# Kernel optimization log

Hardware: AMD Instinct MI355X
Metric: run time of the kernel (lower is better)

The kernel has to match this reference:

```python
import jax, jax.numpy as jnp
import numpy as np

MEM = 128   # mem_dim
K = 4096    # number of object keys (each an array leaf list)
L = 128     # numbers per array
STATS_CAP = 100  # number_stats list capped at 100 entries


def setup_inputs() -> dict:
    key = jax.random.key(0)
    ks = jax.random.split(key, 13)
    s = 0.05
    return {
        "numbers": jax.random.normal(ks[0], (K, L), jnp.float32),
        "w_num": jax.random.normal(ks[1], (MEM,), jnp.float32) * s,
        "b_num": jax.random.normal(ks[2], (MEM,), jnp.float32) * s,
        "W_ih": jax.random.normal(ks[3], (4 * MEM, 2 * MEM), jnp.float32) * s,
        "W_hh": jax.random.normal(ks[4], (4 * MEM, MEM), jnp.float32) * s,
        "b_ih": jax.random.normal(ks[5], (4 * MEM,), jnp.float32) * s,
        "b_hh": jax.random.normal(ks[6], (4 * MEM,), jnp.float32) * s,
        "W_fh": jax.random.normal(ks[7], (MEM, MEM), jnp.float32) * s,
        "b_fh": jax.random.normal(ks[8], (MEM,), jnp.float32) * s,
        "W_iouh": jax.random.normal(ks[9], (3 * MEM, MEM), jnp.float32) * s,
        "b_iouh": jax.random.normal(ks[10], (3 * MEM,), jnp.float32) * s,
        "W_lout": jax.random.normal(ks[11], (MEM, MEM), jnp.float32) * s,
        "b_lout": jax.random.normal(ks[12], (MEM,), jnp.float32) * s,
    }


def _normalize_numbers(x_flat):
    # Replicates embed_number's running number_stats (tie_primitives -> one shared
    # '___default___' stats list, filled in traversal order, capped at 100 entries).
    # The k-th number is normalized by mean/std over the first min(k, 100) numbers
    # (including itself); std division only when len > 3 and std not ~0.
    n = x_flat.shape[0]
    k = jnp.arange(1, n + 1, dtype=jnp.float32)
    cs = jnp.cumsum(x_flat)
    css = jnp.cumsum(x_flat * x_flat)
    cap = jnp.minimum(k, float(STATS_CAP))
    cs_c = jnp.where(k <= STATS_CAP, cs, cs[STATS_CAP - 1])
    css_c = jnp.where(k <= STATS_CAP, css, css[STATS_CAP - 1])
    mean = cs_c / cap
    var = jnp.maximum(css_c / cap - mean * mean, 0.0)
    std = jnp.sqrt(var)
    # torch impl computes stats with numpy -> no gradient flows through them
    mean = jax.lax.stop_gradient(mean)
    std = jax.lax.stop_gradient(std)
    y = x_flat - mean
    use_std = (cap > 3.0) & (std > 1e-8)
    return jnp.where(use_std, y / jnp.where(use_std, std, 1.0), y)


def _forward(numbers, w_num, b_num, W_ih, W_hh, b_ih, b_hh,
             W_fh, b_fh, W_iouh, b_iouh, W_lout, b_lout):
    # --- embed_number: per-leaf (c=0, h = Linear(1, MEM)(norm_num)) ---
    x = _normalize_numbers(numbers.reshape(-1)).reshape(K, L)
    h_num = x[..., None] * w_num + b_num  # [K, L, MEM]

    # --- embed_array: LSTMCell over each array's children; input = cat([c_child, h_child]) ---
    # child_c is always 0 for number leaves.
    def step(carry, h_t):  # h_t: [K, MEM]
        c, h = carry
        xcat = jnp.concatenate([jnp.zeros_like(h_t), h_t], axis=-1)  # [K, 2*MEM]
        gates = xcat @ W_ih.T + b_ih + h @ W_hh.T + b_hh             # [K, 4*MEM]
        i, f, g, o = jnp.split(gates, 4, axis=-1)
        c2 = jax.nn.sigmoid(f) * c + jax.nn.sigmoid(i) * jnp.tanh(g)
        h2 = jax.nn.sigmoid(o) * jnp.tanh(c2)
        return (c2, h2), None

    z = jnp.zeros((K, MEM), numbers.dtype)
    (c_arr, h_arr), _ = jax.lax.scan(step, (z, z), jnp.swapaxes(h_num, 0, 1))
    # c_arr, h_arr: [K, MEM] final states per array child of the root object

    # --- embed_object (root): child-sum Tree-LSTM gating ---
    f_g = jax.nn.sigmoid(h_arr @ W_fh.T + b_fh)             # [K, MEM]
    fc_sum = jnp.sum(f_g * c_arr, axis=0, keepdims=True)    # [1, MEM]
    hs_bar = jnp.sum(h_arr, axis=0, keepdims=True)          # [1, MEM]
    iou = hs_bar @ W_iouh.T + b_iouh
    i, o, u = jnp.split(iou, 3, axis=-1)
    c = jax.nn.sigmoid(i) * jnp.tanh(u) + fc_sum
    h = jax.nn.sigmoid(o) * jnp.tanh(c)
    h_hat = h @ W_lout.T + b_lout
    return jnp.concatenate([c, h_hat], axis=1)  # [1, 2*MEM]


def reference(numbers, w_num, b_num, W_ih, W_hh, b_ih, b_hh,
              W_fh, b_fh, W_iouh, b_iouh, W_lout, b_lout):
    return _forward(numbers, w_num, b_num, W_ih, W_hh, b_ih, b_hh,
                    W_fh, b_fh, W_iouh, b_iouh, W_lout, b_lout)
```

## Files before the change

kernel.cpp:

```cpp
#include <hip/hip_runtime.h>
#include <math.h>

#define L2E 1.4426950408889634f
#define HSTR 136
#define PRS 16

typedef __bf16 bf16x8 __attribute__((ext_vector_type(8)));
typedef float  f32x4  __attribute__((ext_vector_type(4)));

__device__ __forceinline__ float sig2(float y) {
    return __builtin_amdgcn_rcpf(1.0f + __builtin_amdgcn_exp2f(-y));
}

__global__ void prep_kernel(const float* __restrict__ numbers,
                            const float* __restrict__ w_num,
                            const float* __restrict__ b_num,
                            const float* __restrict__ W_ih,
                            const float* __restrict__ b_ih,
                            const float* __restrict__ b_hh,
                            float* __restrict__ ws_base) {
    float* fc_hs    = ws_base;
    float* mean_lut = ws_base + 256;
    float* inv_lut  = ws_base + 356;
    float* Avec     = ws_base + 456;
    float* Bvec     = ws_base + 968;

    if (blockIdx.x == 64) {
        __shared__ float sx[100];
        int tid = threadIdx.x;
        if (tid < 256) fc_hs[tid] = 0.0f;
        if (tid < 100) sx[tid] = numbers[tid];
        __syncthreads();
        if (tid < 100) {
            float s = 0.f, ss = 0.f;
            for (int j = 0; j <= tid; ++j) { float v = sx[j]; s += v; ss += v * v; }
            float cap  = (float)(tid + 1);
            float mean = s / cap;
            float var  = ss / cap - mean * mean;
            if (var < 0.f) var = 0.f;
            float sd = sqrtf(var);
            float inv = (cap > 3.0f && sd > 1e-8f) ? (1.0f / sd) : 1.0f;
            mean_lut[tid] = mean;
            inv_lut[tid]  = inv;
        }
        return;
    }
    int j    = blockIdx.x * 8 + (threadIdx.x >> 6);
    int lane = threadIdx.x & 63;
    const float* row = W_ih + j * 256 + 128;
    float r1 = row[lane], r2 = row[lane + 64];
    float a = r1 * w_num[lane] + r2 * w_num[lane + 64];
    float b = r1 * b_num[lane] + r2 * b_num[lane + 64];
    #pragma unroll
    for (int off = 32; off >= 1; off >>= 1) {
        a += __shfl_xor(a, off);
        b += __shfl_xor(b, off);
    }
    if (lane == 0) {
        float s = (j >= 256 && j < 384) ? (2.0f * L2E) : L2E;
        Avec[j] = a * s;
        Bvec[j] = (b + b_ih[j] + b_hh[j]) * s;
    }
}

__global__ __launch_bounds__(1024, 4) void lstm_kernel(
        const float* __restrict__ numbers, const float* __restrict__ W_hh,
        const float* __restrict__ W_fh,    const float* __restrict__ b_fh,
        const float* __restrict__ mean_lut, const float* __restrict__ inv_lut,
        const float* __restrict__ Avec,     const float* __restrict__ Bvec,
        float* __restrict__ fc_sum, float* __restrict__ hs_bar) {
    __shared__ unsigned short hbuf[2][16 * HSTR];
    __shared__ float xls[128 * 16];
    __shared__ float pbuf[128 * PRS];

    const int tid  = threadIdx.x;
    const int lane = tid & 63;
    const int wave = tid >> 6;
    const bool low = wave < 8;
    const int quad = lane >> 4;
    const int lcol = lane & 15;
    const int m0   = (wave & 7) * 16;
    const int r0   = blockIdx.x * 16;

    for (int i = tid; i < 16 * 128; i += 1024) {
        int row = i >> 7;
        int t   = i & 127;
        int flat = (r0 + row) * 128 + t;
        int ii = (flat < 100) ? flat : 99;
        float v = numbers[flat];
        xls[t * 16 + row] = (v - mean_lut[ii]) * inv_lut[ii];
    }
    for (int i = tid; i < 16 * HSTR; i += 1024) hbuf[0][i] = 0;

    const int g0 = low ? 0 : 1;
    const int g1 = low ? 2 : 3;
    const float s0 = L2E;
    const float s1 = low ? (2.0f * L2E) : L2E;
    bf16x8 bf[2][4];
    #pragma unroll
    for (int gi = 0; gi < 2; ++gi) {
        int g = gi ? g1 : g0;
        float sc = gi ? s1 : s0;
        #pragma unroll
        for (int kk = 0; kk < 4; ++kk) {
            const float* p = W_hh + (g * 128 + m0 + lcol) * 128 + kk * 32 + quad * 8;
            f32x4 w0 = *(const f32x4*)p;
            f32x4 w1 = *(const f32x4*)(p + 4);
            bf16x8 bt;
            #pragma unroll
            for (int q = 0; q < 4; ++q) {
                bt[q]     = (__bf16)(w0[q] * sc);
                bt[q + 4] = (__bf16)(w1[q] * sc);
            }
            bf[gi][kk] = bt;
        }
    }
    float ag[2], bg[2];
    ag[0] = Avec[g0 * 128 + m0 + lcol];  bg[0] = Bvec[g0 * 128 + m0 + lcol];
    ag[1] = Avec[g1 * 128 + m0 + lcol];  bg[1] = Bvec[g1 * 128 + m0 + lcol];

    float c[4]  = {0.f, 0.f, 0.f, 0.f};
    float hf[4] = {0.f, 0.f, 0.f, 0.f};
    __syncthreads();

    for (int t = 0; t < 128; ++t) {
        const unsigned short* hin = hbuf[t & 1];
        unsigned short* hout = hbuf[(t + 1) & 1];
        bf16x8 af[4];
        #pragma unroll
        for (int kk = 0; kk < 4; ++kk)
            af[kk] = *(const bf16x8*)(const void*)(hin + lcol * HSTR + kk * 32 + quad * 8);
        f32x4 xq = *(const f32x4*)(const void*)(xls + t * 16 + quad * 4);
        f32x4 acc[2];
        #pragma unroll
        for (int gi = 0; gi < 2; ++gi) {
            f32x4 a0;
            #pragma unroll
            for (int r = 0; r < 4; ++r) a0[r] = xq[r] * ag[gi] + bg[gi];
            #pragma unroll
            for (int kk = 0; kk < 4; ++kk)
                a0 = __builtin_amdgcn_mfma_f32_16x16x32_bf16(af[kk], bf[gi][kk], a0, 0, 0, 0);
            acc[gi] = a0;
        }
        float sf[4], so[4];
        if (low) {
            f32x4 pv;
            #pragma unroll
            for (int r = 0; r < 4; ++r) {
                float si = sig2(acc[0][r]);
                float tg = 2.0f * sig2(acc[1][r]) - 1.0f;
                pv[r] = si * tg;
            }
            *(f32x4*)(pbuf + (m0 + lcol) * PRS + quad * 4) = pv;
        } else {
            #pragma unroll
            for (int r = 0; r < 4; ++r) {
                sf[r] = sig2(acc[0][r]);
                so[r] = sig2(acc[1][r]);
            }
        }
        __syncthreads();
        if (!low) {
            f32x4 pv = *(const f32x4*)(const void*)(pbuf + (m0 + lcol) * PRS + quad * 4);
            #pragma unroll
            for (int r = 0; r < 4; ++r) {
                float c2 = sf[r] * c[r] + pv[r];
                c[r] = c2;
                float th = 2.0f * sig2(c2 * (2.0f * L2E)) - 1.0f;
                float h = so[r] * th;
                hf[r] = h;
                hout[(quad * 4 + r) * HSTR + m0 + lcol] =
                    __builtin_bit_cast(unsigned short, (__bf16)h);
            }
        }
        __syncthreads();
    }

    if (!low) {
        float v = hf[0] + hf[1] + hf[2] + hf[3];
        v += __shfl_xor(v, 16);
        v += __shfl_xor(v, 32);
        if (lane < 16) atomicAdd(&hs_bar[m0 + lane], v);
        f32x4 facc;
        {
            float bb = b_fh[m0 + lcol] * L2E;
            #pragma unroll
            for (int r = 0; r < 4; ++r) facc[r] = bb;
        }
        #pragma unroll
        for (int kk = 0; kk < 4; ++kk) {
            bf16x8 afr = *(const bf16x8*)(const void*)(hbuf[0] + lcol * HSTR + kk * 32 + quad * 8);
            const float* p = W_fh + (m0 + lcol) * 128 + kk * 32 + quad * 8;
            f32x4 w0 = *(const f32x4*)p;
            f32x4 w1 = *(const f32x4*)(p + 4);
            bf16x8 wt;
            #pragma unroll
            for (int q = 0; q < 4; ++q) {
                wt[q]     = (__bf16)(w0[q] * L2E);
                wt[q + 4] = (__bf16)(w1[q] * L2E);
            }
            facc = __builtin_amdgcn_mfma_f32_16x16x32_bf16(afr, wt, facc, 0, 0, 0);
        }
        float fcv = 0.f;
        #pragma unroll
        for (int r = 0; r < 4; ++r) fcv += sig2(facc[r]) * c[r];
        fcv += __shfl_xor(fcv, 16);
        fcv += __shfl_xor(fcv, 32);
        if (lane < 16) atomicAdd(&fc_sum[m0 + lane], fcv);
    }
}

__global__ void finalize_kernel(const float* __restrict__ fc_sum,
                                const float* __restrict__ hs_bar,
                                const float* __restrict__ W_iouh,
                                const float* __restrict__ b_iouh,
                                const float* __restrict__ W_lout,
                                const float* __restrict__ b_lout,
                                float* __restrict__ out) {
    __shared__ float hsb[128], iou[384], hfin[128];
    int tid = threadIdx.x;
    if (tid < 128) hsb[tid] = hs_bar[tid];
    __syncthreads();
    if (tid < 384) {
        float s = b_iouh[tid];
        const f32x4* row = (const f32x4*)(W_iouh + tid * 128);
        #pragma unroll 8
        for (int m = 0; m < 32; ++m) {
            f32x4 w = row[m];
            s += w[0] * hsb[4*m] + w[1] * hsb[4*m+1] + w[2] * hsb[4*m+2] + w[3] * hsb[4*m+3];
        }
        iou[tid] = s;
    }
    __syncthreads();
    if (tid < 128) {
        float i = iou[tid], o = iou[128 + tid], u = iou[256 + tid];
        float cf = sig2(i * L2E) * (2.0f * sig2(u * 2.0f * L2E) - 1.0f) + fc_sum[tid];
        out[tid] = cf;
        hfin[tid] = sig2(o * L2E) * (2.0f * sig2(cf * 2.0f * L2E) - 1.0f);
    }
    __syncthreads();
    if (tid < 128) {
        float s = b_lout[tid];
        const f32x4* row = (const f32x4*)(W_lout + tid * 128);
        #pragma unroll 8
        for (int m = 0; m < 32; ++m) {
            f32x4 w = row[m];
            s += w[0] * hfin[4*m] + w[1] * hfin[4*m+1] + w[2] * hfin[4*m+2] + w[3] * hfin[4*m+3];
        }
        out[128 + tid] = s;
    }
}

extern "C" void kernel_launch(void* const* d_in, const int* in_sizes, int n_in,
                              void* d_out, int out_size, void* d_ws, size_t ws_size,
                              hipStream_t stream) {
    const float* numbers = (const float*)d_in[0];
    const float* w_num   = (const float*)d_in[1];
    const float* b_num   = (const float*)d_in[2];
    const float* W_ih    = (const float*)d_in[3];
    const float* W_hh    = (const float*)d_in[4];
    const float* b_ih    = (const float*)d_in[5];
    const float* b_hh    = (const float*)d_in[6];
    const float* W_fh    = (const float*)d_in[7];
    const float* b_fh    = (const float*)d_in[8];
    const float* W_iouh  = (const float*)d_in[9];
    const float* b_iouh  = (const float*)d_in[10];
    const float* W_lout  = (const float*)d_in[11];
    const float* b_lout  = (const float*)d_in[12];
    float* out = (float*)d_out;

    float* ws       = (float*)d_ws;
    float* fc_sum   = ws;
    float* hs_bar   = ws + 128;
    float* mean_lut = ws + 256;
    float* inv_lut  = ws + 356;
    float* Avec     = ws + 456;
    float* Bvec     = ws + 968;

    prep_kernel<<<65, 512, 0, stream>>>(numbers, w_num, b_num, W_ih, b_ih, b_hh, ws);
    lstm_kernel<<<256, 1024, 0, stream>>>(numbers, W_hh, W_fh, b_fh,
                                          mean_lut, inv_lut, Avec, Bvec, fc_sum, hs_bar);
    finalize_kernel<<<1, 384, 0, stream>>>(fc_sum, hs_bar, W_iouh, b_iouh, W_lout, b_lout, out);
}
```

Baseline: 218.9 us.

## Compute all four gates per wave redundantly, drop pbuf exchange and one barrier

Each wave now runs MFMAs for all four LSTM gates instead of splitting gates across two wave halves. The two halves divide the four output rows of each tile, so the shared-memory pbuf exchange and one __syncthreads per timestep go away. The gate nonlinearities are also fused, sharing one reciprocal per product. In exchange, MFMA work per wave doubles and register pressure rises from holding 16 weight fragments.

```diff
diff --git a/kernel.cpp b/kernel.cpp
--- a/kernel.cpp
+++ b/kernel.cpp
@@ -3,7 +3,6 @@
 
 #define L2E 1.4426950408889634f
 #define HSTR 136
-#define PRS 16
 
 typedef __bf16 bf16x8 __attribute__((ext_vector_type(8)));
 typedef float  f32x4  __attribute__((ext_vector_type(4)));
@@ -71,12 +70,11 @@
         float* __restrict__ fc_sum, float* __restrict__ hs_bar) {
     __shared__ unsigned short hbuf[2][16 * HSTR];
     __shared__ float xls[128 * 16];
-    __shared__ float pbuf[128 * PRS];
 
     const int tid  = threadIdx.x;
     const int lane = tid & 63;
     const int wave = tid >> 6;
-    const bool low = wave < 8;
+    const int par  = wave >> 3;
     const int quad = lane >> 4;
     const int lcol = lane & 15;
     const int m0   = (wave & 7) * 16;
@@ -92,15 +90,10 @@
     }
     for (int i = tid; i < 16 * HSTR; i += 1024) hbuf[0][i] = 0;
 
-    const int g0 = low ? 0 : 1;
-    const int g1 = low ? 2 : 3;
-    const float s0 = L2E;
-    const float s1 = low ? (2.0f * L2E) : L2E;
-    bf16x8 bf[2][4];
-    #pragma unroll
-    for (int gi = 0; gi < 2; ++gi) {
-        int g = gi ? g1 : g0;
-        float sc = gi ? s1 : s0;
+    bf16x8 bf[4][4];
+    #pragma unroll
+    for (int g = 0; g < 4; ++g) {
+        float sc = (g == 2) ? (2.0f * L2E) : L2E;
         #pragma unroll
         for (int kk = 0; kk < 4; ++kk) {
             const float* p = W_hh + (g * 128 + m0 + lcol) * 128 + kk * 32 + quad * 8;
@@ -112,102 +105,102 @@
                 bt[q]     = (__bf16)(w0[q] * sc);
                 bt[q + 4] = (__bf16)(w1[q] * sc);
             }
-            bf[gi][kk] = bt;
-        }
-    }
-    float ag[2], bg[2];
-    ag[0] = Avec[g0 * 128 + m0 + lcol];  bg[0] = Bvec[g0 * 128 + m0 + lcol];
-    ag[1] = Avec[g1 * 128 + m0 + lcol];  bg[1] = Bvec[g1 * 128 + m0 + lcol];
-
-    float c[4]  = {0.f, 0.f, 0.f, 0.f};
-    float hf[4] = {0.f, 0.f, 0.f, 0.f};
-    __syncthreads();
+            bf[g][kk] = bt;
+        }
+    }
+    float ag[4], bg[4];
+    #pragma unroll
+    for (int g = 0; g < 4; ++g) {
+        ag[g] = Avec[g * 128 + m0 + lcol];
+        bg[g] = Bvec[g * 128 + m0 + lcol];
+    }
+
+    float c0 = 0.f, c1 = 0.f, h0 = 0.f, h1 = 0.f;
+    __syncthreads();
+
+#define ROW_TAIL(R, cS, hS)                                                          \
+    {                                                                                \
+        float e1 = __builtin_amdgcn_exp2f(-aI[R]);                                   \
+        float e2 = __builtin_amdgcn_exp2f(aG[R]);                                    \
+        float pp = (e2 - 1.0f) * __builtin_amdgcn_rcpf((1.0f + e1) * (e2 + 1.0f));   \
+        float sf = sig2(aF[R]);                                                      \
+        float cn = sf * cS + pp;                                                     \
+        cS = cn;                                                                     \
+        float e3 = __builtin_amdgcn_exp2f(cn * (2.0f * L2E));                        \
+        float e4 = __builtin_amdgcn_exp2f(-aO[R]);                                   \
+        hS = (e3 - 1.0f) * __builtin_amdgcn_rcpf((1.0f + e4) * (e3 + 1.0f));         \
+        hout[(quad * 4 + (R)) * HSTR + m0 + lcol] =                                  \
+            __builtin_bit_cast(unsigned short, (__bf16)hS);                          \
+    }
 
     for (int t = 0; t < 128; ++t) {
-        const unsigned short* hin = hbuf[t & 1];
-        unsigned short* hout = hbuf[(t + 1) & 1];
+        const unsigned short* hin  = hbuf[t & 1];
+        unsigned short*       hout = hbuf[(t + 1) & 1];
         bf16x8 af[4];
         #pragma unroll
         for (int kk = 0; kk < 4; ++kk)
             af[kk] = *(const bf16x8*)(const void*)(hin + lcol * HSTR + kk * 32 + quad * 8);
         f32x4 xq = *(const f32x4*)(const void*)(xls + t * 16 + quad * 4);
-        f32x4 acc[2];
-        #pragma unroll
-        for (int gi = 0; gi < 2; ++gi) {
-            f32x4 a0;
-            #pragma unroll
-            for (int r = 0; r < 4; ++r) a0[r] = xq[r] * ag[gi] + bg[gi];
-            #pragma unroll
-            for (int kk = 0; kk < 4; ++kk)
-                a0 = __builtin_amdgcn_mfma_f32_16x16x32_bf16(af[kk], bf[gi][kk], a0, 0, 0, 0);
-            acc[gi] = a0;
-        }
-        float sf[4], so[4];
-        if (low) {
-            f32x4 pv;
-            #pragma unroll
-            for (int r = 0; r < 4; ++r) {
-                float si = sig2(acc[0][r]);
-                float tg = 2.0f * sig2(acc[1][r]) - 1.0f;
-                pv[r] = si * tg;
-            }
-            *(f32x4*)(pbuf + (m0 + lcol) * PRS + quad * 4) = pv;
+
+        f32x4 aI, aG, aF, aO;
+        #pragma unroll
+        for (int r = 0; r < 4; ++r) {
+            aI[r] = xq[r] * ag[0] + bg[0];
+            aG[r] = xq[r] * ag[2] + bg[2];
+            aF[r] = xq[r] * ag[1] + bg[1];
+            aO[r] = xq[r] * ag[3] + bg[3];
+        }
+        #pragma unroll
+        for (int kk = 0; kk < 4; ++kk) {
+            aI = __builtin_amdgcn_mfma_f32_16x16x32_bf16(af[kk], bf[0][kk], aI, 0, 0, 0);
+            aG = __builtin_amdgcn_mfma_f32_16x16x32_bf16(af[kk], bf[2][kk], aG, 0, 0, 0);
+        }
+        #pragma unroll
+        for (int kk = 0; kk < 4; ++kk) {
+            aF = __builtin_amdgcn_mfma_f32_16x16x32_bf16(af[kk], bf[1][kk], aF, 0, 0, 0);
+            aO = __builtin_amdgcn_mfma_f32_16x16x32_bf16(af[kk], bf[3][kk], aO, 0, 0, 0);
+        }
+        if (par == 0) {
+            ROW_TAIL(0, c0, h0)
+            ROW_TAIL(1, c1, h1)
         } else {
-            #pragma unroll
-            for (int r = 0; r < 4; ++r) {
-                sf[r] = sig2(acc[0][r]);
-                so[r] = sig2(acc[1][r]);
-            }
+            ROW_TAIL(2, c0, h0)
+            ROW_TAIL(3, c1, h1)
         }
         __syncthreads();
-        if (!low) {
-            f32x4 pv = *(const f32x4*)(const void*)(pbuf + (m0 + lcol) * PRS + quad * 4);
-            #pragma unroll
-            for (int r = 0; r < 4; ++r) {
-                float c2 = sf[r] * c[r] + pv[r];
-                c[r] = c2;
-                float th = 2.0f * sig2(c2 * (2.0f * L2E)) - 1.0f;
-                float h = so[r] * th;
-                hf[r] = h;
-                hout[(quad * 4 + r) * HSTR + m0 + lcol] =
-                    __builtin_bit_cast(unsigned short, (__bf16)h);
-            }
-        }
-        __syncthreads();
-    }
-
-    if (!low) {
-        float v = hf[0] + hf[1] + hf[2] + hf[3];
-        v += __shfl_xor(v, 16);
-        v += __shfl_xor(v, 32);
-        if (lane < 16) atomicAdd(&hs_bar[m0 + lane], v);
-        f32x4 facc;
-        {
-            float bb = b_fh[m0 + lcol] * L2E;
-            #pragma unroll
-            for (int r = 0; r < 4; ++r) facc[r] = bb;
-        }
-        #pragma unroll
-        for (int kk = 0; kk < 4; ++kk) {
-            bf16x8 afr = *(const bf16x8*)(const void*)(hbuf[0] + lcol * HSTR + kk * 32 + quad * 8);
-            const float* p = W_fh + (m0 + lcol) * 128 + kk * 32 + quad * 8;
-            f32x4 w0 = *(const f32x4*)p;
-            f32x4 w1 = *(const f32x4*)(p + 4);
-            bf16x8 wt;
-            #pragma unroll
-            for (int q = 0; q < 4; ++q) {
-                wt[q]     = (__bf16)(w0[q] * L2E);
-                wt[q + 4] = (__bf16)(w1[q] * L2E);
-            }
-            facc = __builtin_amdgcn_mfma_f32_16x16x32_bf16(afr, wt, facc, 0, 0, 0);
-        }
-        float fcv = 0.f;
-        #pragma unroll
-        for (int r = 0; r < 4; ++r) fcv += sig2(facc[r]) * c[r];
-        fcv += __shfl_xor(fcv, 16);
-        fcv += __shfl_xor(fcv, 32);
-        if (lane < 16) atomicAdd(&fc_sum[m0 + lane], fcv);
-    }
+    }
+#undef ROW_TAIL
+
+    float v = h0 + h1;
+    v += __shfl_xor(v, 16);
+    v += __shfl_xor(v, 32);
+    if (lane < 16) atomicAdd(&hs_bar[m0 + lane], v);
+
+    f32x4 facc;
+    {
+        float bb = b_fh[m0 + lcol] * L2E;
+        #pragma unroll
+        for (int r = 0; r < 4; ++r) facc[r] = bb;
+    }
+    #pragma unroll
+    for (int kk = 0; kk < 4; ++kk) {
+        bf16x8 afr = *(const bf16x8*)(const void*)(hbuf[0] + lcol * HSTR + kk * 32 + quad * 8);
+        const float* p = W_fh + (m0 + lcol) * 128 + kk * 32 + quad * 8;
+        f32x4 w0 = *(const f32x4*)p;
+        f32x4 w1 = *(const f32x4*)(p + 4);
+        bf16x8 wt;
+        #pragma unroll
+        for (int q = 0; q < 4; ++q) {
+            wt[q]     = (__bf16)(w0[q] * L2E);
+            wt[q + 4] = (__bf16)(w1[q] * L2E);
+        }
+        facc = __builtin_amdgcn_mfma_f32_16x16x32_bf16(afr, wt, facc, 0, 0, 0);
+    }
+    float fcv = (par == 0) ? (sig2(facc[0]) * c0 + sig2(facc[1]) * c1)
+                           : (sig2(facc[2]) * c0 + sig2(facc[3]) * c1);
+    fcv += __shfl_xor(fcv, 16);
+    fcv += __shfl_xor(fcv, 32);
+    if (lane < 16) atomicAdd(&fc_sum[m0 + lane], fcv);
 }
 
 __global__ void finalize_kernel(const float* __restrict__ fc_sum,
```

Measured after the change: 298.4 us. +36.3%, slower.
